# Kernel optimization log

Hardware: AMD Instinct MI355X
Metric: run time of the kernel (lower is better)

## Reference

```python
import jax, jax.numpy as jnp
import numpy as np

B, C, H, W = 8, 256, 64, 64
AGENT = 5
SCALE = C ** -0.5


def setup_inputs() -> dict:
    key = jax.random.key(0)
    ks = jax.random.split(key, 10)
    d = {}
    d["supp_feat1"] = jax.random.normal(ks[0], (B, C, H, W), jnp.float32)
    d["supp_feat2"] = jax.random.normal(ks[1], (B, C, H, W), jnp.float32)
    d["supp_mask1"] = jax.random.randint(ks[2], (B, H, W), 0, 2, jnp.int32)
    d["supp_mask2"] = jax.random.randint(ks[3], (B, H, W), 0, 2, jnp.int32)
    d["query_feat"] = jax.random.normal(ks[4], (B, C, H, W), jnp.float32)
    d["query_prediction"] = jax.random.normal(ks[5], (B, 2, H, W), jnp.float32)
    d["Wq"] = jax.random.normal(ks[6], (C, C), jnp.float32) * 0.02
    d["Wk"] = jax.random.normal(ks[7], (C, C), jnp.float32) * 0.02
    d["Wv"] = jax.random.normal(ks[8], (C, C), jnp.float32) * 0.02
    d["part_tokens"] = jax.random.normal(ks[9], (1, AGENT, C), jnp.float32) * 0.001
    return d


def _sinkhorn_masked(cost, col_mask, reg=0.5, n_iter=300):
    # Masked-column Sinkhorn equivalent to ot.sinkhorn on the fg-selected
    # submatrix (uniform marginals), then zero-scattered back. cost: [r, c].
    r = cost.shape[0]
    a = jnp.full((r,), 1.0 / r, cost.dtype)
    b = col_mask / jnp.sum(col_mask)          # 0 on masked cols
    K = jnp.exp(-cost / reg) * col_mask        # kill masked cols

    def body(u, _):
        v = b / jnp.maximum(K.T @ u, 1e-30)
        u_new = a / jnp.maximum(K @ v, 1e-30)
        return u_new, None

    u, _ = jax.lax.scan(body, a, None, length=n_iter)
    v = b / jnp.maximum(K.T @ u, 1e-30)
    return u[:, None] * K * v[None, :]         # transport plan [r, c]


def _supp_to_prototype(feat, mask, Wq, Wk, Wv, part_tokens):
    # mask is at feature resolution, so F.interpolate is identity.
    mf = (mask == 1).astype(feat.dtype)[:, None]                  # [B,1,H,W]
    proto = jnp.sum(feat * mf, axis=(2, 3)) / (jnp.sum(mf, axis=(2, 3)) + 1e-5)  # [B,C]
    proto = proto[:, None, :] + part_tokens                       # [B,A,C]
    q = proto @ Wq.T                                              # [B,A,C]
    sf = (feat * mf).reshape(B, C, H * W).transpose(0, 2, 1)      # [B,HW,C]
    k = sf @ Wk.T
    v = sf @ Wv.T
    attn = jnp.einsum("bac,bnc->ban", q, k)                      # [B,A,HW]
    # torch does (~mask_int).float() * -1e4 == (mask_int + 1) * 1e4
    bias = (mask.reshape(B, -1) + 1).astype(feat.dtype) * 10000.0
    attn = jax.nn.softmax(attn + bias[:, None, :], axis=-1)
    # background cols are exp(-1e4) == 0 in fp32, so attn > 0 <=> mask == 1
    col_mask = (mask.reshape(B, -1) == 1).astype(feat.dtype)      # [B,HW]
    cost = 1.0 - attn                                             # detached in torch
    plan = jax.lax.stop_gradient(jax.vmap(_sinkhorn_masked)(cost, col_mask))
    return proto + jnp.einsum("ban,bnc->bac", plan, v)


def _forward(supp_feat1, supp_feat2, supp_mask1, supp_mask2, query_feat,
             query_prediction, Wq, Wk, Wv, part_tokens):
    p1 = _supp_to_prototype(supp_feat1, supp_mask1, Wq, Wk, Wv, part_tokens)
    p2 = _supp_to_prototype(supp_feat2, supp_mask2, Wq, Wk, Wv, part_tokens)
    curr = jnp.concatenate([p1, p2], axis=1)                      # [B,2A,C]
    fg = jax.nn.softmax(query_prediction, axis=1)[:, 1:2]         # [B,1,H,W]
    fg = jnp.where(fg > 0.7, jnp.asarray(1.0, fg.dtype), fg)
    fg = jnp.where(fg < 0.3, jnp.asarray(0.0, fg.dtype), fg)
    qf = (query_feat * fg).reshape(B, C, H * W).transpose(0, 2, 1)  # [B,HW,C]
    attn = jnp.einsum("bnc,bmc->bnm", curr, qf) * SCALE
    attn = jax.nn.softmax(attn, axis=-1)
    curr = curr + jnp.einsum("bnm,bmc->bnc", attn, qf)
    mem = jnp.concatenate([p1, p2, curr], axis=1)                 # [B,4A,C]
    curr_prototype = jnp.mean(mem, axis=1, keepdims=True)         # [B,1,C]
    return mem, curr_prototype


def reference(supp_feat1, supp_feat2, supp_mask1, supp_mask2, query_feat,
              query_prediction, Wq, Wk, Wv, part_tokens):
    return _forward(supp_feat1, supp_feat2, supp_mask1, supp_mask2, query_feat,
                    query_prediction, Wq, Wk, Wv, part_tokens)
```

## Files before the change

### kernel.cpp

```cpp
#include <hip/hip_runtime.h>
#include <hip/hip_bf16.h>
#include <math.h>

#define HW 4096
#define NC 256
#define NB 8
#define NA 5
#define NIT 24
#define SCL 0.0625f

#define OFF_A     0
#define OFF_PROTO 655360
#define OFF_QK    (OFF_PROTO + 4096)
#define OFF_PS    (OFF_QK + 20480)
#define OFF_W2    (OFF_PS + 20480)
#define OFF_WQK   OFF_W2

__device__ inline float frcp(float x) { return __builtin_amdgcn_rcpf(x); }

template<int NV>
__device__ inline void waveSum(float (&v)[NV]) {
    #pragma unroll
    for (int k = 0; k < NV; ++k) {
        float x = v[k]; int t;
        t = __builtin_amdgcn_update_dpp(0, __float_as_int(x), 0x111, 0xf, 0xf, true); x += __int_as_float(t);
        t = __builtin_amdgcn_update_dpp(0, __float_as_int(x), 0x112, 0xf, 0xf, true); x += __int_as_float(t);
        t = __builtin_amdgcn_update_dpp(0, __float_as_int(x), 0x114, 0xf, 0xf, true); x += __int_as_float(t);
        t = __builtin_amdgcn_update_dpp(0, __float_as_int(x), 0x118, 0xf, 0xf, true); x += __int_as_float(t);
        t = __builtin_amdgcn_update_dpp(0, __float_as_int(x), 0x142, 0xf, 0xf, true); x += __int_as_float(t);
        t = __builtin_amdgcn_update_dpp(0, __float_as_int(x), 0x143, 0xf, 0xf, true); x += __int_as_float(t);
        v[k] = x;
    }
}

template<int NV>
__device__ inline void waveMax(float (&v)[NV]) {
    #pragma unroll
    for (int k = 0; k < NV; ++k) {
        float x = v[k]; int t;
        t = __builtin_amdgcn_update_dpp(__float_as_int(x), __float_as_int(x), 0x111, 0xf, 0xf, false); x = fmaxf(x, __int_as_float(t));
        t = __builtin_amdgcn_update_dpp(__float_as_int(x), __float_as_int(x), 0x112, 0xf, 0xf, false); x = fmaxf(x, __int_as_float(t));
        t = __builtin_amdgcn_update_dpp(__float_as_int(x), __float_as_int(x), 0x114, 0xf, 0xf, false); x = fmaxf(x, __int_as_float(t));
        t = __builtin_amdgcn_update_dpp(__float_as_int(x), __float_as_int(x), 0x118, 0xf, 0xf, false); x = fmaxf(x, __int_as_float(t));
        t = __builtin_amdgcn_update_dpp(__float_as_int(x), __float_as_int(x), 0x142, 0xf, 0xf, false); x = fmaxf(x, __int_as_float(t));
        t = __builtin_amdgcn_update_dpp(__float_as_int(x), __float_as_int(x), 0x143, 0xf, 0xf, false); x = fmaxf(x, __int_as_float(t));
        v[k] = x;
    }
}

template<int NV>
__device__ inline void crossSum4(float (&v)[NV], float* buf, int lane, int wid) {
    waveSum<NV>(v);
    if (lane == 63) {
        #pragma unroll
        for (int k = 0; k < NV; ++k) buf[wid * NV + k] = v[k];
    }
    __syncthreads();
    #pragma unroll
    for (int k = 0; k < NV; ++k)
        v[k] = buf[k] + buf[NV + k] + buf[2 * NV + k] + buf[3 * NV + k];
}

template<int NV>
__device__ inline void crossMax4(float (&v)[NV], float* buf, int lane, int wid) {
    waveMax<NV>(v);
    if (lane == 63) {
        #pragma unroll
        for (int k = 0; k < NV; ++k) buf[wid * NV + k] = v[k];
    }
    __syncthreads();
    #pragma unroll
    for (int k = 0; k < NV; ++k)
        v[k] = fmaxf(fmaxf(buf[k], buf[NV + k]), fmaxf(buf[2 * NV + k], buf[3 * NV + k]));
}

__global__ __launch_bounds__(256) void k_stage1(const float* __restrict__ f1, const float* __restrict__ f2,
                                                const int* __restrict__ m1, const int* __restrict__ m2,
                                                const float* __restrict__ Wq, const float* __restrict__ Wk,
                                                float* __restrict__ ws) {
    __shared__ float buf[8];
    int bid = blockIdx.x, tid = threadIdx.x;
    if (bid < 4096) {
        int lane = tid & 63, wid = tid >> 6;
        int s = bid >> 11, b = (bid >> 8) & 7, c = bid & 255;
        const float* f = s ? f2 : f1;
        const int* m = s ? m2 : m1;
        const float4* fb4 = (const float4*)(f + ((size_t)b * NC + c) * HW);
        const int4* mb4 = (const int4*)(m + b * HW);
        float v2[2] = {0.f, 0.f};
        #pragma unroll
        for (int j = 0; j < 4; ++j) {
            int idx = tid + j * 256;
            float4 v = fb4[idx];
            int4 mm = mb4[idx];
            if (mm.x == 1) { v2[0] += v.x; v2[1] += 1.f; }
            if (mm.y == 1) { v2[0] += v.y; v2[1] += 1.f; }
            if (mm.z == 1) { v2[0] += v.z; v2[1] += 1.f; }
            if (mm.w == 1) { v2[0] += v.w; v2[1] += 1.f; }
        }
        crossSum4<2>(v2, buf, lane, wid);
        if (tid == 0)
            ws[OFF_PROTO + (s * 8 + b) * NC + c] = v2[0] / (v2[1] + 1e-5f);
    } else {
        int c1 = bid - 4096;
        float acc = 0.f;
        #pragma unroll 8
        for (int cp = 0; cp < NC; ++cp)
            acc += Wq[(size_t)cp * NC + c1] * Wk[(size_t)cp * NC + tid];
        ws[OFF_WQK + (size_t)c1 * NC + tid] = acc;
    }
}

__global__ __launch_bounds__(256) void k_attnlogF(const float* __restrict__ f1, const float* __restrict__ f2,
                                                  const float* __restrict__ tok, float* __restrict__ ws) {
    __shared__ float sp3[NA * NC];
    __shared__ float qkp[2][NA * 128];
    __shared__ float qk_l[NA * 128];
    int bid = blockIdx.x, tid = threadIdx.x;
    int ct = bid & 1, nt = (bid >> 1) & 7, sb = bid >> 4;
    int s = sb >> 3, b = sb & 7;
    const float* f = s ? f2 : f1;
    const float* proto = ws + OFF_PROTO + sb * NC;
    for (int i = tid; i < NA * NC; i += 256) sp3[i] = proto[i & 255] + tok[i];
    __syncthreads();
    {
        int cout = tid & 127, ih = tid >> 7;
        const float* wq = ws + OFF_WQK + (size_t)(ih * 128) * NC + ct * 128 + cout;
        const float* sp = sp3 + ih * 128;
        float a0 = 0, a1 = 0, a2 = 0, a3 = 0, a4 = 0;
        #pragma unroll 4
        for (int i = 0; i < 128; ++i) {
            float w = wq[(size_t)i * NC];
            a0 += sp[0 * NC + i] * w; a1 += sp[1 * NC + i] * w; a2 += sp[2 * NC + i] * w;
            a3 += sp[3 * NC + i] * w; a4 += sp[4 * NC + i] * w;
        }
        qkp[ih][0 * 128 + cout] = a0; qkp[ih][1 * 128 + cout] = a1; qkp[ih][2 * 128 + cout] = a2;
        qkp[ih][3 * 128 + cout] = a3; qkp[ih][4 * 128 + cout] = a4;
    }
    __syncthreads();
    for (int i = tid; i < NA * 128; i += 256) qk_l[i] = qkp[0][i] + qkp[1][i];
    __syncthreads();
    int h0 = (nt * 512 + tid * 2) >> 1;
    const float2* fb2 = (const float2*)(f + (size_t)b * NC * HW + (size_t)ct * 128 * HW);
    float2 acc[NA] = {};
    #pragma unroll 4
    for (int k = 0; k < 128; ++k) {
        float2 v = fb2[(size_t)k * 2048 + h0];
        #pragma unroll
        for (int a = 0; a < NA; ++a) {
            float w = qk_l[a * 128 + k];
            acc[a].x += w * v.x; acc[a].y += w * v.y;
        }
    }
    float2* Lp = (float2*)(ws + OFF_A + (size_t)(ct * 16 + sb) * NA * HW);
    #pragma unroll
    for (int a = 0; a < NA; ++a) Lp[a * 2048 + h0] = acc[a];
}

__global__ __launch_bounds__(256) void k_sinkhorn(const int* __restrict__ m1, const int* __restrict__ m2,
                                                  float* __restrict__ ws) {
    __shared__ float buf[2][24];
    int sb = blockIdx.x, tid = threadIdx.x;
    int lane = tid & 63, wid = tid >> 6;
    int s = sb >> 3, b = sb & 7;
    const int* m = (s ? m2 : m1) + b * HW;
    const float4* A4 = (const float4*)(ws + OFF_A);
    const int4* mb4 = (const int4*)m;

    unsigned mbits = 0;
    float K[NA][16];
    #pragma unroll
    for (int j = 0; j < 4; ++j) {
        int idx = tid + j * 256;
        int4 mm = mb4[idx];
        if (mm.x == 1) mbits |= 1u << (4 * j + 0);
        if (mm.y == 1) mbits |= 1u << (4 * j + 1);
        if (mm.z == 1) mbits |= 1u << (4 * j + 2);
        if (mm.w == 1) mbits |= 1u << (4 * j + 3);
        #pragma unroll
        for (int a = 0; a < NA; ++a) {
            float4 l0 = A4[(size_t)(sb * NA + a) * 1024 + idx];
            float4 l1 = A4[(size_t)((16 + sb) * NA + a) * 1024 + idx];
            K[a][4 * j + 0] = l0.x + l1.x; K[a][4 * j + 1] = l0.y + l1.y;
            K[a][4 * j + 2] = l0.z + l1.z; K[a][4 * j + 3] = l0.w + l1.w;
        }
    }
    float r[NA];
    #pragma unroll
    for (int a = 0; a < NA; ++a) {
        float mx = -3.0e38f;
        #pragma unroll
        for (int j = 0; j < 16; ++j)
            if ((mbits >> j) & 1) mx = fmaxf(mx, K[a][j]);
        r[a] = mx;
    }
    crossMax4<NA>(r, buf[0], lane, wid);
    float rs6[6];
    #pragma unroll
    for (int a = 0; a < NA; ++a) {
        float sum = 0.f;
        #pragma unroll
        for (int j = 0; j < 16; ++j) {
            float e = ((mbits >> j) & 1) ? expf(K[a][j] - r[a]) : 0.f;
            K[a][j] = e; sum += e;
        }
        rs6[a] = sum;
    }
    rs6[5] = (float)__popc(mbits);
    crossSum4<6>(rs6, buf[1], lane, wid);
    float inv_cnt = frcp(rs6[5]);
    #pragma unroll
    for (int a = 0; a < NA; ++a) {
        float irs = frcp(rs6[a]);
        #pragma unroll
        for (int j = 0; j < 16; ++j) {
            float attn = K[a][j] * irs;
            K[a][j] = ((mbits >> j) & 1) ? expf(2.f * attn - 2.f) : 0.f;
        }
    }
    float u[NA];
    #pragma unroll
    for (int a = 0; a < NA; ++a) u[a] = 0.2f;
    for (int it = 0; it < NIT; ++it) {
        float part[NA] = {0, 0, 0, 0, 0};
        #pragma unroll
        for (int j = 0; j < 16; ++j) {
            float d = 0.f;
            #pragma unroll
            for (int a = 0; a < NA; ++a) d += K[a][j] * u[a];
            float t = inv_cnt * frcp(fmaxf(d, 1e-30f));
            #pragma unroll
            for (int a = 0; a < NA; ++a) part[a] += K[a][j] * t;
        }
        crossSum4<NA>(part, buf[it & 1], lane, wid);
        #pragma unroll
        for (int a = 0; a < NA; ++a) u[a] = 0.2f * frcp(fmaxf(part[a], 1e-30f));
    }
    float4* Pb4 = (float4*)(ws + OFF_A) + (size_t)sb * NA * 1024;
    #pragma unroll
    for (int j4 = 0; j4 < 4; ++j4) {
        int idx = tid + j4 * 256;
        float tcol[4];
        #pragma unroll
        for (int k = 0; k < 4; ++k) {
            int j = 4 * j4 + k;
            float d = 0.f;
            #pragma unroll
            for (int a = 0; a < NA; ++a) d += K[a][j] * u[a];
            tcol[k] = inv_cnt * frcp(fmaxf(d, 1e-30f));
        }
        #pragma unroll
        for (int a = 0; a < NA; ++a) {
            float4 o;
            o.x = u[a] * K[a][4 * j4 + 0] * tcol[0];
            o.y = u[a] * K[a][4 * j4 + 1] * tcol[1];
            o.z = u[a] * K[a][4 * j4 + 2] * tcol[2];
            o.w = u[a] * K[a][4 * j4 + 3] * tcol[3];
            Pb4[a * 1024 + idx] = o;
        }
    }
}

__global__ __launch_bounds__(256) void k_ps(const float* __restrict__ f1, const float* __restrict__ f2,
                                            float* __restrict__ ws) {
    __shared__ float buf[20];
    int bid = blockIdx.x, tid = threadIdx.x;
    int lane = tid & 63, wid = tid >> 6;
    int s = bid >> 11, b = (bid >> 8) & 7, c = bid & 255;
    const float* f = s ? f2 : f1;
    int sb = s * 8 + b;
    const float4* fb4 = (const float4*)(f + ((size_t)b * NC + c) * HW);
    const float4* Pb4 = (const float4*)(ws + OFF_A) + (size_t)sb * NA * 1024;
    float acc[NA] = {0, 0, 0, 0, 0};
    #pragma unroll
    for (int j = 0; j < 4; ++j) {
        int idx = tid + j * 256;
        float4 v = fb4[idx];
        #pragma unroll
        for (int a = 0; a < NA; ++a) {
            float4 p = Pb4[a * 1024 + idx];
            acc[a] += p.x * v.x + p.y * v.y + p.z * v.z + p.w * v.w;
        }
    }
    crossSum4<NA>(acc, buf, lane, wid);
    if (tid == 0) {
        float* ps = ws + OFF_PS + sb * NA * NC;
        #pragma unroll
        for (int a = 0; a < NA; ++a) ps[a * NC + c] = acc[a];
    }
}

__global__ __launch_bounds__(256) void k_outproto(const float* __restrict__ Wv, const float* __restrict__ tok,
                                                  float* __restrict__ ws, float* __restrict__ out) {
    __shared__ float wv_l[16][NC + 1];
    __shared__ float ps_l[NA * NC];
    __shared__ float part[80][2];
    int bid = blockIdx.x, tid = threadIdx.x;
    int ctile = bid & 15, sb = bid >> 4;
    int s = sb >> 3, b = sb & 7;
    int c0 = ctile * 16;
    const float4* wv4 = (const float4*)(Wv + (size_t)c0 * NC);
    for (int t = tid; t < 1024; t += 256) {
        int r = t >> 6, q = t & 63;
        float4 v = wv4[(size_t)r * 64 + q];
        wv_l[r][4 * q + 0] = v.x; wv_l[r][4 * q + 1] = v.y;
        wv_l[r][4 * q + 2] = v.z; wv_l[r][4 * q + 3] = v.w;
    }
    const float* ps = ws + OFF_PS + sb * NA * NC;
    for (int i = tid; i < NA * NC; i += 256) ps_l[i] = ps[i];
    __syncthreads();
    if (tid < 160) {
        int o = tid >> 1, seg = tid & 1;
        int a = o >> 4, r = o & 15;
        const float* pa = ps_l + a * NC + seg * 128;
        const float* wr = &wv_l[r][seg * 128];
        float d = 0.f;
        #pragma unroll 8
        for (int i = 0; i < 128; ++i) d += pa[i] * wr[i];
        part[o][seg] = d;
    }
    __syncthreads();
    if (tid < 80) {
        int a = tid >> 4, r = tid & 15;
        int c = c0 + r;
        out[(size_t)b * 20 * NC + (s * NA + a) * NC + c] =
            ws[OFF_PROTO + sb * NC + c] + tok[a * NC + c] + part[tid][0] + part[tid][1];
    }
}

__global__ __launch_bounds__(256) void k_attn2log(const float* __restrict__ qf, const float* __restrict__ out,
                                                  float* __restrict__ ws) {
    __shared__ float sc_l[NA * 128];
    int bid = blockIdx.x, tid = threadIdx.x;
    int ig = bid & 1, ct = (bid >> 1) & 1, nt = (bid >> 2) & 7, b = bid >> 5;
    const float* cb = out + (size_t)b * 20 * NC + ig * NA * NC + ct * 128;
    for (int i = tid; i < NA * 128; i += 256) sc_l[i] = cb[(i >> 7) * NC + (i & 127)];
    __syncthreads();
    int h0 = (nt * 512 + tid * 2) >> 1;
    const float2* fb2 = (const float2*)(qf + (size_t)b * NC * HW + (size_t)ct * 128 * HW);
    float2 acc[NA] = {};
    #pragma unroll 4
    for (int k = 0; k < 128; ++k) {
        float2 v = fb2[(size_t)k * 2048 + h0];
        #pragma unroll
        for (int ii = 0; ii < NA; ++ii) {
            float w = sc_l[ii * 128 + k];
            acc[ii].x += w * v.x; acc[ii].y += w * v.y;
        }
    }
    float2* pp = (float2*)(ws + OFF_A + (size_t)(((ct * 2 + ig) * 8 + b) * NA) * HW);
    #pragma unroll
    for (int ii = 0; ii < NA; ++ii) pp[ii * 2048 + h0] = acc[ii];
}

__global__ __launch_bounds__(256) void k_softmax2(const float* __restrict__ qp, float* __restrict__ ws) {
    __shared__ float buf[2][8];
    int row = blockIdx.x, tid = threadIdx.x;
    int lane = tid & 63, wid = tid >> 6;
    int b = row / 10, i = row - b * 10;
    int ig = i / NA, ii = i - ig * NA;
    const float4* pA = (const float4*)(ws + OFF_A) + (size_t)((ig * 8 + b) * NA + ii) * 1024;
    const float4* pB = (const float4*)(ws + OFF_A) + (size_t)(((2 + ig) * 8 + b) * NA + ii) * 1024;
    const float4* qp0 = (const float4*)(qp + (size_t)b * 2 * HW);
    const float4* qp1 = qp0 + 1024;
    float4 lg[4], fgv[4];
    float mx[1] = {-3.0e38f};
    #pragma unroll
    for (int j = 0; j < 4; ++j) {
        int idx = tid + j * 256;
        float4 a = pA[idx], c = pB[idx];
        float4 p0 = qp0[idx], p1 = qp1[idx];
        float4 fg;
        fg.x = 1.f / (1.f + expf(p0.x - p1.x));
        fg.y = 1.f / (1.f + expf(p0.y - p1.y));
        fg.z = 1.f / (1.f + expf(p0.z - p1.z));
        fg.w = 1.f / (1.f + expf(p0.w - p1.w));
        fg.x = fg.x > 0.7f ? 1.f : (fg.x < 0.3f ? 0.f : fg.x);
        fg.y = fg.y > 0.7f ? 1.f : (fg.y < 0.3f ? 0.f : fg.y);
        fg.z = fg.z > 0.7f ? 1.f : (fg.z < 0.3f ? 0.f : fg.z);
        fg.w = fg.w > 0.7f ? 1.f : (fg.w < 0.3f ? 0.f : fg.w);
        fgv[j] = fg;
        lg[j].x = (a.x + c.x) * SCL * fg.x;
        lg[j].y = (a.y + c.y) * SCL * fg.y;
        lg[j].z = (a.z + c.z) * SCL * fg.z;
        lg[j].w = (a.w + c.w) * SCL * fg.w;
        mx[0] = fmaxf(mx[0], fmaxf(fmaxf(lg[j].x, lg[j].y), fmaxf(lg[j].z, lg[j].w)));
    }
    crossMax4<1>(mx, buf[0], lane, wid);
    float sum[1] = {0.f};
    #pragma unroll
    for (int j = 0; j < 4; ++j) {
        lg[j].x = expf(lg[j].x - mx[0]); lg[j].y = expf(lg[j].y - mx[0]);
        lg[j].z = expf(lg[j].z - mx[0]); lg[j].w = expf(lg[j].w - mx[0]);
        sum[0] += lg[j].x + lg[j].y + lg[j].z + lg[j].w;
    }
    crossSum4<1>(sum, buf[1], lane, wid);
    float inv = frcp(sum[0]);
    float4* w24 = (float4*)(ws + OFF_W2) + (size_t)row * 1024;
    #pragma unroll
    for (int j = 0; j < 4; ++j) {
        int idx = tid + j * 256;
        float4 o;
        o.x = lg[j].x * inv * fgv[j].x;
        o.y = lg[j].y * inv * fgv[j].y;
        o.z = lg[j].z * inv * fgv[j].z;
        o.w = lg[j].w * inv * fgv[j].w;
        w24[idx] = o;
    }
}

__global__ __launch_bounds__(256) void k_apply2(const float* __restrict__ qf, float* __restrict__ ws,
                                                float* __restrict__ out) {
    __shared__ float buf[4 * 40];
    int bid = blockIdx.x, tid = threadIdx.x;
    int lane = tid & 63, wid = tid >> 6;
    int b = bid >> 6, cg = bid & 63;
    int c0 = cg * 4;
    const float4* qf4 = (const float4*)(qf + (size_t)b * NC * HW);
    const float4* w24 = (const float4*)(ws + OFF_W2) + (size_t)b * 10 * 1024;
    float acc[40] = {};
    #pragma unroll
    for (int j = 0; j < 4; ++j) {
        int idx = tid + j * 256;
        float4 wv[10];
        #pragma unroll
        for (int i = 0; i < 10; ++i) wv[i] = w24[i * 1024 + idx];
        #pragma unroll
        for (int cc = 0; cc < 4; ++cc) {
            float4 v = qf4[(size_t)(c0 + cc) * 1024 + idx];
            #pragma unroll
            for (int i = 0; i < 10; ++i)
                acc[cc * 10 + i] += wv[i].x * v.x + wv[i].y * v.y + wv[i].z * v.z + wv[i].w * v.w;
        }
    }
    waveSum<40>(acc);
    if (lane == 63) {
        #pragma unroll
        for (int k = 0; k < 40; ++k) buf[wid * 40 + k] = acc[k];
    }
    __syncthreads();
    if (tid == 0) {
        float* ob = out + (size_t)b * 20 * NC;
        #pragma unroll
        for (int cc = 0; cc < 4; ++cc) {
            float s = 0.f;
            #pragma unroll
            for (int i = 0; i < 10; ++i) {
                float d = buf[cc * 10 + i] + buf[40 + cc * 10 + i]
                        + buf[80 + cc * 10 + i] + buf[120 + cc * 10 + i];
                float base = ob[i * NC + c0 + cc];
                float r = base + d;
                ob[(10 + i) * NC + c0 + cc] = r;
                s += base + r;
            }
            out[40960 + b * NC + c0 + cc] = s * 0.05f;
        }
    }
}

extern "C" void kernel_launch(void* const* d_in, const int* in_sizes, int n_in,
                              void* d_out, int out_size, void* d_ws, size_t ws_size,
                              hipStream_t stream) {
    const float* f1  = (const float*)d_in[0];
    const float* f2  = (const float*)d_in[1];
    const int*   m1  = (const int*)d_in[2];
    const int*   m2  = (const int*)d_in[3];
    const float* qf  = (const float*)d_in[4];
    const float* qp  = (const float*)d_in[5];
    const float* Wq  = (const float*)d_in[6];
    const float* Wk  = (const float*)d_in[7];
    const float* Wv  = (const float*)d_in[8];
    const float* tok = (const float*)d_in[9];
    float* out = (float*)d_out;
    float* ws  = (float*)d_ws;

    k_stage1<<<4352, 256, 0, stream>>>(f1, f2, m1, m2, Wq, Wk, ws);
    k_attnlogF<<<256, 256, 0, stream>>>(f1, f2, tok, ws);
    k_sinkhorn<<<16, 256, 0, stream>>>(m1, m2, ws);
    k_ps<<<4096, 256, 0, stream>>>(f1, f2, ws);
    k_outproto<<<256, 256, 0, stream>>>(Wv, tok, ws, out);
    k_attn2log<<<256, 256, 0, stream>>>(qf, out, ws);
    k_softmax2<<<80, 256, 0, stream>>>(qp, ws);
    k_apply2<<<512, 256, 0, stream>>>(qf, ws, out);
}
```

Baseline: 141.3 us.

## Compute full-channel attention logits per block, dropping split-C partial sums

The attention-logit kernel no longer splits the 256 channels into two halves written as separate partial logit buffers. Each block now computes the full q·Wk projection over all 256 channels and reduces over all channels for 256 pixels, writing a single logit buffer. The Sinkhorn kernel then reads one buffer instead of loading and adding two partials. This halves partial-result traffic and the extra load pass, but each block does twice the serial channel loop, uses scalar instead of float2 loads, and the grid keeps the same block count with longer per-block work.

```diff
diff --git a/kernel.cpp b/kernel.cpp
--- a/kernel.cpp
+++ b/kernel.cpp
@@ -11,8 +11,7 @@
 
 #define OFF_A     0
 #define OFF_PROTO 655360
-#define OFF_QK    (OFF_PROTO + 4096)
-#define OFF_PS    (OFF_QK + 20480)
+#define OFF_PS    (OFF_PROTO + 4096 + 20480)
 #define OFF_W2    (OFF_PS + 20480)
 #define OFF_WQK   OFF_W2
 
@@ -114,47 +113,39 @@
 __global__ __launch_bounds__(256) void k_attnlogF(const float* __restrict__ f1, const float* __restrict__ f2,
                                                   const float* __restrict__ tok, float* __restrict__ ws) {
     __shared__ float sp3[NA * NC];
-    __shared__ float qkp[2][NA * 128];
-    __shared__ float qk_l[NA * 128];
-    int bid = blockIdx.x, tid = threadIdx.x;
-    int ct = bid & 1, nt = (bid >> 1) & 7, sb = bid >> 4;
+    __shared__ float qk_l[NA * NC];
+    int bid = blockIdx.x, tid = threadIdx.x;
+    int nt = bid & 15, sb = bid >> 4;
     int s = sb >> 3, b = sb & 7;
     const float* f = s ? f2 : f1;
     const float* proto = ws + OFF_PROTO + sb * NC;
     for (int i = tid; i < NA * NC; i += 256) sp3[i] = proto[i & 255] + tok[i];
     __syncthreads();
     {
-        int cout = tid & 127, ih = tid >> 7;
-        const float* wq = ws + OFF_WQK + (size_t)(ih * 128) * NC + ct * 128 + cout;
-        const float* sp = sp3 + ih * 128;
+        const float* wq = ws + OFF_WQK + tid;
         float a0 = 0, a1 = 0, a2 = 0, a3 = 0, a4 = 0;
-        #pragma unroll 4
-        for (int i = 0; i < 128; ++i) {
-            float w = wq[(size_t)i * NC];
-            a0 += sp[0 * NC + i] * w; a1 += sp[1 * NC + i] * w; a2 += sp[2 * NC + i] * w;
-            a3 += sp[3 * NC + i] * w; a4 += sp[4 * NC + i] * w;
-        }
-        qkp[ih][0 * 128 + cout] = a0; qkp[ih][1 * 128 + cout] = a1; qkp[ih][2 * 128 + cout] = a2;
-        qkp[ih][3 * 128 + cout] = a3; qkp[ih][4 * 128 + cout] = a4;
-    }
-    __syncthreads();
-    for (int i = tid; i < NA * 128; i += 256) qk_l[i] = qkp[0][i] + qkp[1][i];
-    __syncthreads();
-    int h0 = (nt * 512 + tid * 2) >> 1;
-    const float2* fb2 = (const float2*)(f + (size_t)b * NC * HW + (size_t)ct * 128 * HW);
-    float2 acc[NA] = {};
+        #pragma unroll 8
+        for (int ci = 0; ci < NC; ++ci) {
+            float w = wq[(size_t)ci * NC];
+            a0 += sp3[0 * NC + ci] * w; a1 += sp3[1 * NC + ci] * w; a2 += sp3[2 * NC + ci] * w;
+            a3 += sp3[3 * NC + ci] * w; a4 += sp3[4 * NC + ci] * w;
+        }
+        qk_l[0 * NC + tid] = a0; qk_l[1 * NC + tid] = a1; qk_l[2 * NC + tid] = a2;
+        qk_l[3 * NC + tid] = a3; qk_l[4 * NC + tid] = a4;
+    }
+    __syncthreads();
+    int n = nt * 256 + tid;
+    const float* fb = f + (size_t)b * NC * HW + n;
+    float acc[NA] = {};
     #pragma unroll 4
-    for (int k = 0; k < 128; ++k) {
-        float2 v = fb2[(size_t)k * 2048 + h0];
-        #pragma unroll
-        for (int a = 0; a < NA; ++a) {
-            float w = qk_l[a * 128 + k];
-            acc[a].x += w * v.x; acc[a].y += w * v.y;
-        }
-    }
-    float2* Lp = (float2*)(ws + OFF_A + (size_t)(ct * 16 + sb) * NA * HW);
-    #pragma unroll
-    for (int a = 0; a < NA; ++a) Lp[a * 2048 + h0] = acc[a];
+    for (int c = 0; c < NC; ++c) {
+        float v = fb[(size_t)c * HW];
+        #pragma unroll
+        for (int a = 0; a < NA; ++a) acc[a] += qk_l[a * NC + c] * v;
+    }
+    float* Lb = ws + OFF_A + (size_t)sb * NA * HW;
+    #pragma unroll
+    for (int a = 0; a < NA; ++a) Lb[a * HW + n] = acc[a];
 }
 
 __global__ __launch_bounds__(256) void k_sinkhorn(const int* __restrict__ m1, const int* __restrict__ m2,
@@ -164,7 +155,7 @@
     int lane = tid & 63, wid = tid >> 6;
     int s = sb >> 3, b = sb & 7;
     const int* m = (s ? m2 : m1) + b * HW;
-    const float4* A4 = (const float4*)(ws + OFF_A);
+    const float4* A4 = (const float4*)(ws + OFF_A) + (size_t)sb * NA * 1024;
     const int4* mb4 = (const int4*)m;
 
     unsigned mbits = 0;
@@ -179,10 +170,9 @@
         if (mm.w == 1) mbits |= 1u << (4 * j + 3);
         #pragma unroll
         for (int a = 0; a < NA; ++a) {
-            float4 l0 = A4[(size_t)(sb * NA + a) * 1024 + idx];
-            float4 l1 = A4[(size_t)((16 + sb) * NA + a) * 1024 + idx];
-            K[a][4 * j + 0] = l0.x + l1.x; K[a][4 * j + 1] = l0.y + l1.y;
-            K[a][4 * j + 2] = l0.z + l1.z; K[a][4 * j + 3] = l0.w + l1.w;
+            float4 l0 = A4[a * 1024 + idx];
+            K[a][4 * j + 0] = l0.x; K[a][4 * j + 1] = l0.y;
+            K[a][4 * j + 2] = l0.z; K[a][4 * j + 3] = l0.w;
         }
     }
     float r[NA];
```

Result: slower. 146.8 us (+3.9%).
